# Kernel tuning notes

Hardware: AMD Instinct MI355X
Metric: run time of the kernel (lower is better)

## Reference

```python
import jax, jax.numpy as jnp
import numpy as np

B, N, F, T, O, E = 4, 30000, 32, 12, 64, 480000


def setup_inputs() -> dict:
    key = jax.random.key(0)
    ks = jax.random.split(key, 20)
    s = 0.05
    inp = {
        "X": jax.random.normal(ks[0], (B, N, F, T), dtype=jnp.float32),
        "edge_index": jax.random.randint(ks[1], (2, E), 0, N, dtype=jnp.int64),
        # GCNConv weights for the three gates (num_layers=1 -> single conv each)
        "Wg_z": jax.random.normal(ks[2], (F, O), dtype=jnp.float32) * s,
        "bg_z": jnp.zeros((O,), jnp.float32),
        "Wg_r": jax.random.normal(ks[3], (F, O), dtype=jnp.float32) * s,
        "bg_r": jnp.zeros((O,), jnp.float32),
        "Wg_h": jax.random.normal(ks[4], (F, O), dtype=jnp.float32) * s,
        "bg_h": jnp.zeros((O,), jnp.float32),
        # gate Linear(2*O, O) weights
        "Wl_z": jax.random.normal(ks[5], (2 * O, O), dtype=jnp.float32) * s,
        "bl_z": jnp.zeros((O,), jnp.float32),
        "Wl_r": jax.random.normal(ks[6], (2 * O, O), dtype=jnp.float32) * s,
        "bl_r": jnp.zeros((O,), jnp.float32),
        "Wl_h": jax.random.normal(ks[7], (2 * O, O), dtype=jnp.float32) * s,
        "bl_h": jnp.zeros((O,), jnp.float32),
        # A3TGCN per-period attention and final readout Linear(O, T)
        "att": jax.random.normal(ks[8], (T,), dtype=jnp.float32),
        "W_out": jax.random.normal(ks[9], (O, T), dtype=jnp.float32) * s,
        "b_out": jnp.zeros((T,), jnp.float32),
    }
    return inp


def reference(X, edge_index, Wg_z, bg_z, Wg_r, bg_r, Wg_h, bg_h,
              Wl_z, bl_z, Wl_r, bl_r, Wl_h, bl_h, att, W_out, b_out):
    src, dst = edge_index[0], edge_index[1]
    n = X.shape[1]
    # GCN symmetric normalization with self-loops: deg = in-degree + 1
    deg = jnp.zeros((n,), X.dtype).at[dst].add(1.0) + 1.0
    dis = jax.lax.rsqrt(deg)  # deg^{-1/2}
    edge_norm = (dis[src] * dis[dst])[None, :, None]  # [1,E,1]
    self_norm = (dis * dis)[None, :, None]            # [1,N,1]

    def gcn_conv(x, W, b):  # x: [B,N,F] -> [B,N,O]
        xw = jnp.einsum('bnf,fo->bno', x, W)
        agg = jnp.zeros_like(xw).at[:, dst, :].add(xw[:, src, :] * edge_norm)
        return agg + xw * self_norm + b

    H0 = jnp.zeros((X.shape[0], n, Wg_z.shape[1]), X.dtype)  # H defaults to zeros
    probs = jax.nn.softmax(att)

    def step(acc, inp):
        x_t, p = inp  # x_t: [B,N,F]
        Z = jax.nn.sigmoid(jnp.concatenate([gcn_conv(x_t, Wg_z, bg_z), H0], -1) @ Wl_z + bl_z)
        R = jax.nn.sigmoid(jnp.concatenate([gcn_conv(x_t, Wg_r, bg_r), H0], -1) @ Wl_r + bl_r)
        Ht = jnp.tanh(jnp.concatenate([gcn_conv(x_t, Wg_h, bg_h), H0 * R], -1) @ Wl_h + bl_h)
        Hn = Z * H0 + (1.0 - Z) * Ht
        return acc + p * Hn, None

    Xt = jnp.moveaxis(X, -1, 0)  # [T,B,N,F]
    H_acc, _ = jax.lax.scan(step, jnp.zeros_like(H0), (Xt, probs))
    # TemporalGNN head: ReLU + Linear(O, periods)
    return jax.nn.relu(H_acc) @ W_out + b_out  # [B,N,T]
```

## Files before the change

### kernel.cpp

```cpp
#include <hip/hip_runtime.h>
#include <hip/hip_bf16.h>
#include <hip/hip_fp16.h>


#define FDIM 32
#define TDIM 12
#define ODIM 64
#define BDIM 4

typedef _Float16 half8v __attribute__((ext_vector_type(8)));
typedef float float4v __attribute__((ext_vector_type(4)));

__global__ void k_count(const int* __restrict__ dst, int* __restrict__ counts, int E) {
    int e = blockIdx.x * 256 + threadIdx.x;
    if (e < E) atomicAdd(&counts[dst[e]], 1);
}

__global__ __launch_bounds__(1024) void k_scan(const int* __restrict__ counts,
                                               int* __restrict__ offsets,
                                               float* __restrict__ dis, int N) {
    __shared__ int wsum[16];
    __shared__ int sCarry;
    const int tid = threadIdx.x;
    const int lane = tid & 63;
    const int wv = tid >> 6;
    if (tid == 0) sCarry = 0;
    __syncthreads();
    for (int base = 0; base < N; base += 1024) {
        int i = base + tid;
        int v = (i < N) ? (counts[i] + 1) : 0;
        int s = v;
        for (int off = 1; off < 64; off <<= 1) {
            int t = __shfl_up(s, off, 64);
            if (lane >= off) s += t;
        }
        if (lane == 63) wsum[wv] = s;
        __syncthreads();
        if (wv == 0 && lane < 16) {
            int ws = wsum[lane];
            for (int off = 1; off < 16; off <<= 1) {
                int t = __shfl_up(ws, off, 64);
                if (lane >= off) ws += t;
            }
            wsum[lane] = ws;
        }
        __syncthreads();
        int carry = sCarry;
        int wpre = (wv > 0) ? wsum[wv - 1] : 0;
        if (i < N) {
            offsets[i] = carry + wpre + s - v;
            dis[i] = 1.0f / sqrtf((float)v);
        }
        __syncthreads();
        if (tid == 0) sCarry = carry + wsum[15];
        __syncthreads();
    }
    if (tid == 0) offsets[N] = sCarry;
}

__global__ void k_self(const int* __restrict__ offsets, const float* __restrict__ dis,
                       int* __restrict__ fill, int2* __restrict__ csr, int N) {
    int n = blockIdx.x * 256 + threadIdx.x;
    if (n < N) {
        float d = dis[n];
        csr[offsets[n]] = make_int2(n, __float_as_int(d * d));
        fill[n] = 1;
    }
}

__global__ void k_scatter(const int* __restrict__ src, const int* __restrict__ dst,
                          const int* __restrict__ offsets, int* __restrict__ fill,
                          const float* __restrict__ dis,
                          int2* __restrict__ csr, int E) {
    int e = blockIdx.x * 256 + threadIdx.x;
    if (e < E) {
        int s = src[e], d = dst[e];
        int pos = offsets[d] + atomicAdd(&fill[d], 1);
        csr[pos] = make_int2(s, __float_as_int(dis[s] * dis[d]));
    }
}

__global__ void k_prep(const float* __restrict__ Wg_z, const float* __restrict__ bg_z,
                       const float* __restrict__ Wl_z, const float* __restrict__ bl_z,
                       const float* __restrict__ Wg_h, const float* __restrict__ bg_h,
                       const float* __restrict__ Wl_h, const float* __restrict__ bl_h,
                       const float* __restrict__ att,
                       float* __restrict__ Wz, float* __restrict__ bz,
                       float* __restrict__ Wh, float* __restrict__ bh,
                       float* __restrict__ probs) {
    int tid = threadIdx.x;
    for (int i = tid; i < FDIM * ODIM; i += 256) {
        int f = i >> 6, o = i & 63;
        float az = 0.f, ah = 0.f;
        for (int k = 0; k < ODIM; k++) {
            az += Wg_z[f * ODIM + k] * Wl_z[k * ODIM + o];
            ah += Wg_h[f * ODIM + k] * Wl_h[k * ODIM + o];
        }
        Wz[i] = az;
        Wh[i] = ah;
    }
    if (tid < ODIM) {
        float az = bl_z[tid], ah = bl_h[tid];
        for (int k = 0; k < ODIM; k++) {
            az += bg_z[k] * Wl_z[k * ODIM + tid];
            ah += bg_h[k] * Wl_h[k * ODIM + tid];
        }
        bz[tid] = az;
        bh[tid] = ah;
    }
    if (tid == 0) {
        float m = -1e30f;
        for (int t = 0; t < TDIM; t++) m = fmaxf(m, att[t]);
        float e[TDIM], s = 0.f;
        for (int t = 0; t < TDIM; t++) { e[t] = expf(att[t] - m); s += e[t]; }
        for (int t = 0; t < TDIM; t++) probs[t] = e[t] / s;
    }
}

__global__ __launch_bounds__(256) void k_cvt(const float4* __restrict__ in,
                                             uint2* __restrict__ out, int n4) {
    int i = blockIdx.x * 256 + threadIdx.x;
    const int stride = gridDim.x * 256;
    for (; i < n4; i += stride) {
        const float4 v = in[i];
        __half2 h0 = __floats2half2_rn(v.x, v.y);
        __half2 h1 = __floats2half2_rn(v.z, v.w);
        uint2 u;
        u.x = *reinterpret_cast<unsigned*>(&h0);
        u.y = *reinterpret_cast<unsigned*>(&h1);
        out[i] = u;
    }
}

__device__ __forceinline__ float sigm(float x) { return 1.f / (1.f + __expf(-x)); }
__device__ __forceinline__ float tanhfast(float x) { return 1.f - 2.f / (1.f + __expf(2.f * x)); }

#define HPACC(mhI, v, hs0, hs1, hs2, hs3)                                      \
    {                                                                          \
        __half2 mh_ = *(__half2*)&(mhI);                                       \
        hs0 = __hfma2(mh_, *(__half2*)&(v).x, hs0);                            \
        hs1 = __hfma2(mh_, *(__half2*)&(v).y, hs1);                            \
        hs2 = __hfma2(mh_, *(__half2*)&(v).z, hs2);                            \
        hs3 = __hfma2(mh_, *(__half2*)&(v).w, hs3);                            \
    }

#define HFLUSH(hs0, hs1, hs2, hs3)                                             \
    {                                                                          \
        float2 t_;                                                             \
        t_ = __half22float2(hs0); a0 += t_.x; a1 += t_.y;                      \
        t_ = __half22float2(hs1); a2 += t_.x; a3 += t_.y;                      \
        t_ = __half22float2(hs2); a4 += t_.x; a5 += t_.y;                      \
        t_ = __half22float2(hs3); a6 += t_.x; a7 += t_.y;                      \
        hs0 = hzero; hs1 = hzero; hs2 = hzero; hs3 = hzero;                    \
    }

#define GLOADH(dst, mvar, slot)                                                \
    {                                                                          \
        int s_ = __shfl(esrc, (slot), 64);                                     \
        (mvar) = __shfl(hmi, (slot), 64);                                      \
        (dst) = Xh[(rowB + (unsigned)s_) * 48u + lanec];                       \
    }

#define LOADB(dst, Wsrc, jt)                                                   \
    {                                                                          \
        _Pragma("unroll") for (int r_ = 0; r_ < 8; r_++)                       \
            dst[r_] = (_Float16)Wsrc[(kg * 8 + r_) * ODIM + (jt) * 16 + c];    \
    }

#define EPI(qv, dzv, dhv, bzv, bhv)                                            \
    {                                                                          \
        float s_ = 0.f;                                                        \
        {  float zf_ = dzv[0] + bzv, hf_ = dhv[0] + bhv;                       \
           s_ += pr0 * (1.f - sigm(zf_)) * tanhfast(hf_); }                    \
        {  float zf_ = dzv[1] + bzv, hf_ = dhv[1] + bhv;                       \
           s_ += pr1 * (1.f - sigm(zf_)) * tanhfast(hf_); }                    \
        {  float zf_ = dzv[2] + bzv, hf_ = dhv[2] + bhv;                       \
           s_ += pr2 * (1.f - sigm(zf_)) * tanhfast(hf_); }                    \
        {  float zf_ = dzv[3] + bzv, hf_ = dhv[3] + bhv;                       \
           s_ += pr3 * (1.f - sigm(zf_)) * tanhfast(hf_); }                    \
        s_ += __shfl_xor(s_, 16, 64);                                          \
        s_ += __shfl_xor(s_, 32, 64);                                          \
        qv = s_;                                                               \
    }

__global__ __launch_bounds__(256, 4) void k_main_w(
    const uint4* __restrict__ Xh, const int* __restrict__ offs,
    const int2* __restrict__ csr,
    const float* __restrict__ Wz, const float* __restrict__ bz,
    const float* __restrict__ Wh, const float* __restrict__ bh,
    const float* __restrict__ probs, const float* __restrict__ Wout,
    const float* __restrict__ bout, float* __restrict__ out, int N) {
    __shared__ float sY[4][16 * 36 + 4];

    const int tid = threadIdx.x;
    const int wv = tid >> 6;
    const int lane = tid & 63;
    const int lanec = lane < 47 ? lane : 47;
    const int c = lane & 15;
    const int kg = lane >> 4;

    half8v wzf0, wzf1, wzf2, wzf3, whf0, whf1, whf2, whf3;
    LOADB(wzf0, Wz, 0) LOADB(wzf1, Wz, 1) LOADB(wzf2, Wz, 2) LOADB(wzf3, Wz, 3)
    LOADB(whf0, Wh, 0) LOADB(whf1, Wh, 1) LOADB(whf2, Wh, 2) LOADB(whf3, Wh, 3)
    half8v wo0, wo1;
#pragma unroll
    for (int r_ = 0; r_ < 8; r_++) {
        wo0[r_] = (_Float16)((c < TDIM) ? Wout[(kg * 8 + r_) * TDIM + c] : 0.f);
        wo1[r_] = (_Float16)((c < TDIM) ? Wout[(32 + kg * 8 + r_) * TDIM + c] : 0.f);
    }
    const float bz0 = bz[c], bz1 = bz[16 + c], bz2 = bz[32 + c], bz3 = bz[48 + c];
    const float bh0 = bh[c], bh1 = bh[16 + c], bh2 = bh[32 + c], bh3 = bh[48 + c];
    const float pr0 = (kg * 4 + 0 < TDIM) ? probs[kg * 4 + 0] : 0.f;
    const float pr1 = (kg * 4 + 1 < TDIM) ? probs[kg * 4 + 1] : 0.f;
    const float pr2 = (kg * 4 + 2 < TDIM) ? probs[kg * 4 + 2] : 0.f;
    const float pr3 = (kg * 4 + 3 < TDIM) ? probs[kg * 4 + 3] : 0.f;
    const float bo = (lane < TDIM) ? bout[lane] : 0.f;
    const __half2 hzero = __float2half2_rn(0.f);

    float* __restrict__ sy = sY[wv];
    const int strideT = gridDim.x * 4;
    const int totalTasks = N * BDIM;

    int task0 = blockIdx.x * 4 + wv;
    if (task0 >= totalTasks) return;
    int b = task0 / N;
    int n = task0 - b * N;

    while (true) {
        const unsigned rowB = (unsigned)b * (unsigned)N;
        const int beg = offs[n], end = offs[n + 1];

        float a0 = 0.f, a1 = 0.f, a2 = 0.f, a3 = 0.f,
              a4 = 0.f, a5 = 0.f, a6 = 0.f, a7 = 0.f;
        __half2 hA0 = hzero, hA1 = hzero, hA2 = hzero, hA3 = hzero;
        __half2 hB0 = hzero, hB1 = hzero, hB2 = hzero, hB3 = hzero;
        for (int ebase = beg; ebase < end; ebase += 64) {
            const int wcnt = min(64, end - ebase);
            int esrc = 0;
            int hmi = 0;
            if (ebase + lane < end) {
                const int2 e = csr[ebase + lane];
                esrc = e.x;
                const float m = __int_as_float(e.y);
                __half2 mh = __floats2half2_rn(m, m);
                hmi = *(int*)&mh;
            }
            int j = 0;
            for (; j + 8 <= wcnt; j += 8) {
                uint4 x0, x1, x2, x3, x4, x5, x6, x7;
                int m0, m1, m2, m3, m4, m5, m6, m7;
                GLOADH(x0, m0, j + 0); GLOADH(x1, m1, j + 1);
                GLOADH(x2, m2, j + 2); GLOADH(x3, m3, j + 3);
                GLOADH(x4, m4, j + 4); GLOADH(x5, m5, j + 5);
                GLOADH(x6, m6, j + 6); GLOADH(x7, m7, j + 7);
                HPACC(m0, x0, hA0, hA1, hA2, hA3);
                HPACC(m1, x1, hA0, hA1, hA2, hA3);
                HPACC(m2, x2, hA0, hA1, hA2, hA3);
                HPACC(m3, x3, hA0, hA1, hA2, hA3);
                HPACC(m4, x4, hB0, hB1, hB2, hB3);
                HPACC(m5, x5, hB0, hB1, hB2, hB3);
                HPACC(m6, x6, hB0, hB1, hB2, hB3);
                HPACC(m7, x7, hB0, hB1, hB2, hB3);
                HFLUSH(hA0, hA1, hA2, hA3);
                HFLUSH(hB0, hB1, hB2, hB3);
            }
            for (; j < wcnt; j++) {
                uint4 xv;
                int mv;
                GLOADH(xv, mv, j);
                HPACC(mv, xv, hA0, hA1, hA2, hA3);
            }
            HFLUSH(hA0, hA1, hA2, hA3);
        }

        if (lane < 48) {
            int flat = lane * 8;
            int f = flat / 12;
            int t = flat - f * 12;
#pragma unroll
            for (int k = 0; k < 8; k++) {
                float av = (k == 0) ? a0 : (k == 1) ? a1 : (k == 2) ? a2 :
                           (k == 3) ? a3 : (k == 4) ? a4 : (k == 5) ? a5 :
                           (k == 6) ? a6 : a7;
                sy[t * 36 + f] = av;
                t++;
                if (t == TDIM) { t = 0; f++; }
            }
        }

        half8v af;
        if (c < TDIM) {
            const float4* yp = (const float4*)&sy[c * 36 + kg * 8];
            const float4 y0 = yp[0];
            const float4 y1 = yp[1];
            af[0] = (_Float16)y0.x; af[1] = (_Float16)y0.y;
            af[2] = (_Float16)y0.z; af[3] = (_Float16)y0.w;
            af[4] = (_Float16)y1.x; af[5] = (_Float16)y1.y;
            af[6] = (_Float16)y1.z; af[7] = (_Float16)y1.w;
        } else {
            af[0] = (_Float16)0.f; af[1] = (_Float16)0.f;
            af[2] = (_Float16)0.f; af[3] = (_Float16)0.f;
            af[4] = (_Float16)0.f; af[5] = (_Float16)0.f;
            af[6] = (_Float16)0.f; af[7] = (_Float16)0.f;
        }

        const float4v zero4 = {0.f, 0.f, 0.f, 0.f};
        float4v dz0 = __builtin_amdgcn_mfma_f32_16x16x32_f16(af, wzf0, zero4, 0, 0, 0);
        float4v dz1 = __builtin_amdgcn_mfma_f32_16x16x32_f16(af, wzf1, zero4, 0, 0, 0);
        float4v dz2 = __builtin_amdgcn_mfma_f32_16x16x32_f16(af, wzf2, zero4, 0, 0, 0);
        float4v dz3 = __builtin_amdgcn_mfma_f32_16x16x32_f16(af, wzf3, zero4, 0, 0, 0);
        float4v dh0 = __builtin_amdgcn_mfma_f32_16x16x32_f16(af, whf0, zero4, 0, 0, 0);
        float4v dh1 = __builtin_amdgcn_mfma_f32_16x16x32_f16(af, whf1, zero4, 0, 0, 0);
        float4v dh2 = __builtin_amdgcn_mfma_f32_16x16x32_f16(af, whf2, zero4, 0, 0, 0);
        float4v dh3 = __builtin_amdgcn_mfma_f32_16x16x32_f16(af, whf3, zero4, 0, 0, 0);

        float q0, q1, q2, q3;
        EPI(q0, dz0, dh0, bz0, bh0)
        EPI(q1, dz1, dh1, bz1, bh1)
        EPI(q2, dz2, dh2, bz2, bh2)
        EPI(q3, dz3, dh3, bz3, bh3)
        const float accOwn = (kg == 0) ? q0 : (kg == 1) ? q1 : (kg == 2) ? q2 : q3;

        const float r = fmaxf(accOwn, 0.f);
        half8v ra0, ra1;
#pragma unroll
        for (int j = 0; j < 8; j++) {
            ra0[j] = (_Float16)__shfl(r, (kg << 3) + j, 64);
            ra1[j] = (_Float16)__shfl(r, 32 + (kg << 3) + j, 64);
        }
        float4v dro = __builtin_amdgcn_mfma_f32_16x16x32_f16(ra0, wo0, zero4, 0, 0, 0);
        dro = __builtin_amdgcn_mfma_f32_16x16x32_f16(ra1, wo1, dro, 0, 0, 0);
        if (lane < TDIM)
            out[(rowB + (unsigned)n) * TDIM + lane] = dro[0] + bo;

        n += strideT;
        if (n >= N) { n -= N; b++; }
        if (b >= BDIM) break;
    }
}

__global__ __launch_bounds__(384) void k_main_f(
    const float* __restrict__ X, const int* __restrict__ offsets,
    const int2* __restrict__ csr, const float* __restrict__ dis,
    const float* __restrict__ Wz, const float* __restrict__ bz,
    const float* __restrict__ Wh, const float* __restrict__ bh,
    const float* __restrict__ probs, const float* __restrict__ Wout,
    const float* __restrict__ bout, float* __restrict__ out, int N) {
    const int tid = threadIdx.x;
    const int lane = tid & 63;

    __shared__ float4 sY4[BDIM][96];
    __shared__ float sAcc[BDIM][ODIM];
    __shared__ float sWout[ODIM * TDIM];
    __shared__ float sBout[TDIM];

    for (int i = tid; i < ODIM * TDIM; i += 384) sWout[i] = Wout[i];
    if (tid < TDIM) sBout[tid] = bout[tid];

    const int o = tid & 63;
    const int w = tid >> 6;
    float wzr[FDIM], whr[FDIM];
#pragma unroll
    for (int f = 0; f < FDIM; f++) {
        wzr[f] = Wz[f * ODIM + o];
        whr[f] = Wh[f * ODIM + o];
    }
    const float bzo = bz[o], bho = bh[o];
    const int t0 = w, t1 = w + 6;
    const float p0 = probs[t0], p1 = probs[t1];

    const int b = tid / 96;
    const int q = tid - b * 96;
    const float4* __restrict__ Xq = (const float4*)X;
    const unsigned rowBase = (unsigned)b * (unsigned)N;

    for (int n = blockIdx.x; n < N; n += gridDim.x) {
        if (tid < BDIM * ODIM) ((float*)sAcc)[tid] = 0.f;

        const int beg = offsets[n], end = offsets[n + 1];
        float4 A0 = make_float4(0.f, 0.f, 0.f, 0.f);
        float4 A1 = A0, A2 = A0, A3 = A0;

        for (int ebase = beg; ebase < end; ebase += 64) {
            const int cnt2 = min(64, end - ebase);
            int esrc = 0;
            float enm = 0.f;
            if (ebase + lane < end) {
                const int2 e = csr[ebase + lane];
                esrc = e.x;
                enm = __int_as_float(e.y);
            }
            int j = 0;
            for (; j + 4 <= cnt2; j += 4) {
                const int s0 = __shfl(esrc, j + 0, 64), s1 = __shfl(esrc, j + 1, 64);
                const int s2 = __shfl(esrc, j + 2, 64), s3 = __shfl(esrc, j + 3, 64);
                const float m0 = __shfl(enm, j + 0, 64), m1 = __shfl(enm, j + 1, 64);
                const float m2 = __shfl(enm, j + 2, 64), m3 = __shfl(enm, j + 3, 64);
                const float4 u0 = Xq[(rowBase + s0) * 96u + q];
                const float4 u1 = Xq[(rowBase + s1) * 96u + q];
                const float4 u2 = Xq[(rowBase + s2) * 96u + q];
                const float4 u3 = Xq[(rowBase + s3) * 96u + q];
                A0.x += m0 * u0.x; A0.y += m0 * u0.y; A0.z += m0 * u0.z; A0.w += m0 * u0.w;
                A1.x += m1 * u1.x; A1.y += m1 * u1.y; A1.z += m1 * u1.z; A1.w += m1 * u1.w;
                A2.x += m2 * u2.x; A2.y += m2 * u2.y; A2.z += m2 * u2.z; A2.w += m2 * u2.w;
                A3.x += m3 * u3.x; A3.y += m3 * u3.y; A3.z += m3 * u3.z; A3.w += m3 * u3.w;
            }
            for (; j < cnt2; j++) {
                const int s = __shfl(esrc, j, 64);
                const float m = __shfl(enm, j, 64);
                const float4 u = Xq[(rowBase + s) * 96u + q];
                A0.x += m * u.x; A0.y += m * u.y; A0.z += m * u.z; A0.w += m * u.w;
            }
        }
        A0.x += (A1.x + A2.x) + A3.x;
        A0.y += (A1.y + A2.y) + A3.y;
        A0.z += (A1.z + A2.z) + A3.z;
        A0.w += (A1.w + A2.w) + A3.w;
        sY4[b][q] = A0;
        __syncthreads();

#pragma unroll
        for (int bb = 0; bb < BDIM; bb++) {
            const float* yb = (const float*)sY4[bb];
            float z0 = bzo, z1 = bzo, h0 = bho, h1 = bho;
#pragma unroll
            for (int f = 0; f < FDIM; f++) {
                float ya = yb[f * TDIM + t0];
                float yc = yb[f * TDIM + t1];
                z0 += ya * wzr[f]; h0 += ya * whr[f];
                z1 += yc * wzr[f]; h1 += yc * whr[f];
            }
            float contrib = p0 * (1.f - sigm(z0)) * tanhfast(h0)
                          + p1 * (1.f - sigm(z1)) * tanhfast(h1);
            atomicAdd(&sAcc[bb][o], contrib);
        }
        __syncthreads();

        if (tid < BDIM * TDIM) {
            int ob = tid / TDIM, jj = tid - ob * TDIM;
            float v = sBout[jj];
#pragma unroll
            for (int o2 = 0; o2 < ODIM; o2++) {
                v += fmaxf(sAcc[ob][o2], 0.f) * sWout[o2 * TDIM + jj];
            }
            out[(unsigned)(ob * N + n) * TDIM + jj] = v;
        }
        __syncthreads();
    }
}

extern "C" void kernel_launch(void* const* d_in, const int* in_sizes, int n_in,
                              void* d_out, int out_size, void* d_ws, size_t ws_size,
                              hipStream_t stream) {
    const float* X    = (const float*)d_in[0];
    const int*   ei   = (const int*)d_in[1];
    const float* Wg_z = (const float*)d_in[2];
    const float* bg_z = (const float*)d_in[3];
    const float* Wg_h = (const float*)d_in[6];
    const float* bg_h = (const float*)d_in[7];
    const float* Wl_z = (const float*)d_in[8];
    const float* bl_z = (const float*)d_in[9];
    const float* Wl_h = (const float*)d_in[12];
    const float* bl_h = (const float*)d_in[13];
    const float* att  = (const float*)d_in[14];
    const float* Wout = (const float*)d_in[15];
    const float* bout = (const float*)d_in[16];
    float* out = (float*)d_out;

    const int E = in_sizes[1] / 2;
    const int N = in_sizes[0] / (BDIM * FDIM * TDIM);
    const size_t xElems = (size_t)BDIM * N * FDIM * TDIM;
    const size_t xhBytes = xElems * 2;
    const size_t csrBytes = (size_t)(E + N) * 8;
    const size_t restBytes = (size_t)N * 4 * 4 + 64 + csrBytes + 20000;
    const bool useH = ws_size >= xhBytes + restBytes;

    char* wp = (char*)d_ws;
    uint2* Xh = nullptr;
    if (useH) { Xh = (uint2*)wp; wp += xhBytes; }
    int* counts   = (int*)wp;   wp += (size_t)N * 4;
    int* fill     = (int*)wp;   wp += (size_t)N * 4;
    int* offs     = (int*)wp;   wp += (size_t)(N + 4) * 4;
    float* dis    = (float*)wp; wp += (size_t)N * 4;
    int2* csr     = (int2*)wp;  wp += csrBytes;
    float* Wz     = (float*)wp; wp += FDIM * ODIM * 4;
    float* Wh     = (float*)wp; wp += FDIM * ODIM * 4;
    float* bz     = (float*)wp; wp += ODIM * 4;
    float* bh     = (float*)wp; wp += ODIM * 4;
    float* probs  = (float*)wp; wp += 16 * 4;

    hipMemsetAsync(counts, 0, (size_t)N * 4, stream);

    k_prep<<<1, 256, 0, stream>>>(Wg_z, bg_z, Wl_z, bl_z, Wg_h, bg_h, Wl_h, bl_h,
                                  att, Wz, bz, Wh, bh, probs);
    if (useH) {
        const int n4 = (int)(xElems / 4);
        k_cvt<<<2048, 256, 0, stream>>>((const float4*)X, Xh, n4);
    }
    k_count<<<(E + 255) / 256, 256, 0, stream>>>(ei + E, counts, E);
    k_scan<<<1, 1024, 0, stream>>>(counts, offs, dis, N);
    k_self<<<(N + 255) / 256, 256, 0, stream>>>(offs, dis, fill, csr, N);
    k_scatter<<<(E + 255) / 256, 256, 0, stream>>>(ei, ei + E, offs, fill, dis, csr, E);

    if (useH) {
        k_main_w<<<2048, 256, 0, stream>>>((const uint4*)Xh, offs, csr,
                                           Wz, bz, Wh, bh, probs, Wout, bout, out, N);
    } else {
        int nB = N < 2048 ? N : 2048;
        k_main_f<<<nB, 384, 0, stream>>>(X, offs, csr, dis, Wz, bz, Wh, bh,
                                         probs, Wout, bout, out, N);
    }
}
```

Baseline: 413.2 us.

## Store half2 edge norms in CSR and use scalar edge loads in gather

The CSR build now stores each edge norm as a packed half2 instead of a float, so the gather loop no longer converts it per edge. In the warp kernel the node and offsets are made wave-uniform with readfirstlane, and edges are read directly from the CSR (likely as scalar loads) instead of a coalesced per-lane load followed by shuffles. The epilogue merges the sigmoid and tanh divisions into one reciprocal. This trades shuffle and conversion work for uniform memory reads and a slightly different numeric form, and the float fallback kernel now decodes half norms, which adds some rounding.

```diff
diff --git a/kernel.cpp b/kernel.cpp
--- a/kernel.cpp
+++ b/kernel.cpp
@@ -63,7 +63,9 @@
     int n = blockIdx.x * 256 + threadIdx.x;
     if (n < N) {
         float d = dis[n];
-        csr[offsets[n]] = make_int2(n, __float_as_int(d * d));
+        float nm = d * d;
+        __half2 mh = __floats2half2_rn(nm, nm);
+        csr[offsets[n]] = make_int2(n, *(int*)&mh);
         fill[n] = 1;
     }
 }
@@ -76,7 +78,9 @@
     if (e < E) {
         int s = src[e], d = dst[e];
         int pos = offsets[d] + atomicAdd(&fill[d], 1);
-        csr[pos] = make_int2(s, __float_as_int(dis[s] * dis[d]));
+        float nm = dis[s] * dis[d];
+        __half2 mh = __floats2half2_rn(nm, nm);
+        csr[pos] = make_int2(s, *(int*)&mh);
     }
 }
 
@@ -137,7 +141,8 @@
 
 #define HPACC(mhI, v, hs0, hs1, hs2, hs3)                                      \
     {                                                                          \
-        __half2 mh_ = *(__half2*)&(mhI);                                       \
+        int mi_ = (mhI);                                                       \
+        __half2 mh_ = *(__half2*)&mi_;                                         \
         hs0 = __hfma2(mh_, *(__half2*)&(v).x, hs0);                            \
         hs1 = __hfma2(mh_, *(__half2*)&(v).y, hs1);                            \
         hs2 = __hfma2(mh_, *(__half2*)&(v).z, hs2);                            \
@@ -154,13 +159,6 @@
         hs0 = hzero; hs1 = hzero; hs2 = hzero; hs3 = hzero;                    \
     }
 
-#define GLOADH(dst, mvar, slot)                                                \
-    {                                                                          \
-        int s_ = __shfl(esrc, (slot), 64);                                     \
-        (mvar) = __shfl(hmi, (slot), 64);                                      \
-        (dst) = Xh[(rowB + (unsigned)s_) * 48u + lanec];                       \
-    }
-
 #define LOADB(dst, Wsrc, jt)                                                   \
     {                                                                          \
         _Pragma("unroll") for (int r_ = 0; r_ < 8; r_++)                       \
@@ -170,14 +168,22 @@
 #define EPI(qv, dzv, dhv, bzv, bhv)                                            \
     {                                                                          \
         float s_ = 0.f;                                                        \
-        {  float zf_ = dzv[0] + bzv, hf_ = dhv[0] + bhv;                       \
-           s_ += pr0 * (1.f - sigm(zf_)) * tanhfast(hf_); }                    \
-        {  float zf_ = dzv[1] + bzv, hf_ = dhv[1] + bhv;                       \
-           s_ += pr1 * (1.f - sigm(zf_)) * tanhfast(hf_); }                    \
-        {  float zf_ = dzv[2] + bzv, hf_ = dhv[2] + bhv;                       \
-           s_ += pr2 * (1.f - sigm(zf_)) * tanhfast(hf_); }                    \
-        {  float zf_ = dzv[3] + bzv, hf_ = dhv[3] + bhv;                       \
-           s_ += pr3 * (1.f - sigm(zf_)) * tanhfast(hf_); }                    \
+        {  const float zf_ = dzv[0] + bzv, hf_ = dhv[0] + bhv;                 \
+           const float u_ = __expf(-zf_), v_ = __expf(2.f * hf_);              \
+           s_ += pr0 * u_ * (v_ - 1.f) *                                       \
+                 __builtin_amdgcn_rcpf((1.f + u_) * (1.f + v_)); }             \
+        {  const float zf_ = dzv[1] + bzv, hf_ = dhv[1] + bhv;                 \
+           const float u_ = __expf(-zf_), v_ = __expf(2.f * hf_);              \
+           s_ += pr1 * u_ * (v_ - 1.f) *                                       \
+                 __builtin_amdgcn_rcpf((1.f + u_) * (1.f + v_)); }             \
+        {  const float zf_ = dzv[2] + bzv, hf_ = dhv[2] + bhv;                 \
+           const float u_ = __expf(-zf_), v_ = __expf(2.f * hf_);              \
+           s_ += pr2 * u_ * (v_ - 1.f) *                                       \
+                 __builtin_amdgcn_rcpf((1.f + u_) * (1.f + v_)); }             \
+        {  const float zf_ = dzv[3] + bzv, hf_ = dhv[3] + bhv;                 \
+           const float u_ = __expf(-zf_), v_ = __expf(2.f * hf_);              \
+           s_ += pr3 * u_ * (v_ - 1.f) *                                       \
+                 __builtin_amdgcn_rcpf((1.f + u_) * (1.f + v_)); }             \
         s_ += __shfl_xor(s_, 16, 64);                                          \
         s_ += __shfl_xor(s_, 32, 64);                                          \
         qv = s_;                                                               \
@@ -227,51 +233,45 @@
     int n = task0 - b * N;
 
     while (true) {
-        const unsigned rowB = (unsigned)b * (unsigned)N;
-        const int beg = offs[n], end = offs[n + 1];
+        const int bs = __builtin_amdgcn_readfirstlane(b);
+        const int ns = __builtin_amdgcn_readfirstlane(n);
+        const unsigned rowB = (unsigned)bs * (unsigned)N;
+        const int begS = __builtin_amdgcn_readfirstlane(offs[ns]);
+        const int endS = __builtin_amdgcn_readfirstlane(offs[ns + 1]);
 
         float a0 = 0.f, a1 = 0.f, a2 = 0.f, a3 = 0.f,
               a4 = 0.f, a5 = 0.f, a6 = 0.f, a7 = 0.f;
         __half2 hA0 = hzero, hA1 = hzero, hA2 = hzero, hA3 = hzero;
         __half2 hB0 = hzero, hB1 = hzero, hB2 = hzero, hB3 = hzero;
-        for (int ebase = beg; ebase < end; ebase += 64) {
-            const int wcnt = min(64, end - ebase);
-            int esrc = 0;
-            int hmi = 0;
-            if (ebase + lane < end) {
-                const int2 e = csr[ebase + lane];
-                esrc = e.x;
-                const float m = __int_as_float(e.y);
-                __half2 mh = __floats2half2_rn(m, m);
-                hmi = *(int*)&mh;
-            }
-            int j = 0;
-            for (; j + 8 <= wcnt; j += 8) {
-                uint4 x0, x1, x2, x3, x4, x5, x6, x7;
-                int m0, m1, m2, m3, m4, m5, m6, m7;
-                GLOADH(x0, m0, j + 0); GLOADH(x1, m1, j + 1);
-                GLOADH(x2, m2, j + 2); GLOADH(x3, m3, j + 3);
-                GLOADH(x4, m4, j + 4); GLOADH(x5, m5, j + 5);
-                GLOADH(x6, m6, j + 6); GLOADH(x7, m7, j + 7);
-                HPACC(m0, x0, hA0, hA1, hA2, hA3);
-                HPACC(m1, x1, hA0, hA1, hA2, hA3);
-                HPACC(m2, x2, hA0, hA1, hA2, hA3);
-                HPACC(m3, x3, hA0, hA1, hA2, hA3);
-                HPACC(m4, x4, hB0, hB1, hB2, hB3);
-                HPACC(m5, x5, hB0, hB1, hB2, hB3);
-                HPACC(m6, x6, hB0, hB1, hB2, hB3);
-                HPACC(m7, x7, hB0, hB1, hB2, hB3);
-                HFLUSH(hA0, hA1, hA2, hA3);
-                HFLUSH(hB0, hB1, hB2, hB3);
-            }
-            for (; j < wcnt; j++) {
-                uint4 xv;
-                int mv;
-                GLOADH(xv, mv, j);
-                HPACC(mv, xv, hA0, hA1, hA2, hA3);
-            }
+        int j = begS;
+        for (; j + 8 <= endS; j += 8) {
+            const int2 e0 = csr[j + 0], e1 = csr[j + 1], e2 = csr[j + 2], e3 = csr[j + 3];
+            const int2 e4 = csr[j + 4], e5 = csr[j + 5], e6 = csr[j + 6], e7 = csr[j + 7];
+            const uint4 x0 = Xh[(rowB + (unsigned)e0.x) * 48u + lanec];
+            const uint4 x1 = Xh[(rowB + (unsigned)e1.x) * 48u + lanec];
+            const uint4 x2 = Xh[(rowB + (unsigned)e2.x) * 48u + lanec];
+            const uint4 x3 = Xh[(rowB + (unsigned)e3.x) * 48u + lanec];
+            const uint4 x4 = Xh[(rowB + (unsigned)e4.x) * 48u + lanec];
+            const uint4 x5 = Xh[(rowB + (unsigned)e5.x) * 48u + lanec];
+            const uint4 x6 = Xh[(rowB + (unsigned)e6.x) * 48u + lanec];
+            const uint4 x7 = Xh[(rowB + (unsigned)e7.x) * 48u + lanec];
+            HPACC(e0.y, x0, hA0, hA1, hA2, hA3);
+            HPACC(e1.y, x1, hA0, hA1, hA2, hA3);
+            HPACC(e2.y, x2, hA0, hA1, hA2, hA3);
+            HPACC(e3.y, x3, hA0, hA1, hA2, hA3);
+            HPACC(e4.y, x4, hB0, hB1, hB2, hB3);
+            HPACC(e5.y, x5, hB0, hB1, hB2, hB3);
+            HPACC(e6.y, x6, hB0, hB1, hB2, hB3);
+            HPACC(e7.y, x7, hB0, hB1, hB2, hB3);
             HFLUSH(hA0, hA1, hA2, hA3);
-        }
+            HFLUSH(hB0, hB1, hB2, hB3);
+        }
+        for (; j < endS; ++j) {
+            const int2 e = csr[j];
+            const uint4 xv = Xh[(rowB + (unsigned)e.x) * 48u + lanec];
+            HPACC(e.y, xv, hA0, hA1, hA2, hA3);
+        }
+        HFLUSH(hA0, hA1, hA2, hA3);
 
         if (lane < 48) {
             int flat = lane * 8;
@@ -324,9 +324,9 @@
         const float r = fmaxf(accOwn, 0.f);
         half8v ra0, ra1;
 #pragma unroll
-        for (int j = 0; j < 8; j++) {
-            ra0[j] = (_Float16)__shfl(r, (kg << 3) + j, 64);
-            ra1[j] = (_Float16)__shfl(r, 32 + (kg << 3) + j, 64);
+        for (int j2 = 0; j2 < 8; j2++) {
+            ra0[j2] = (_Float16)__shfl(r, (kg << 3) + j2, 64);
+            ra1[j2] = (_Float16)__shfl(r, 32 + (kg << 3) + j2, 64);
         }
         float4v dro = __builtin_amdgcn_mfma_f32_16x16x32_f16(ra0, wo0, zero4, 0, 0, 0);
         dro = __builtin_amdgcn_mfma_f32_16x16x32_f16(ra1, wo1, dro, 0, 0, 0);
@@ -388,7 +388,8 @@
             if (ebase + lane < end) {
                 const int2 e = csr[ebase + lane];
                 esrc = e.x;
-                enm = __int_as_float(e.y);
+                int ey = e.y;
+                enm = __half22float2(*(__half2*)&ey).x;
             }
             int j = 0;
             for (; j + 4 <= cnt2; j += 4) {
```

After: 377.6 us. 8.6% less time.
